# Performance work log

Measured on AMD Instinct MI355X. Metric: run time of the kernel, lower is better.

Reference implementation:

```python
import math
import jax, jax.numpy as jnp
import numpy as np

B, C_S, C_V = 32768, 256, 128
H = max(C_S, C_V)          # c_hidden
RES_B, RES_A = 4, 5        # SO3_Grid(lmax=1, mmax=1): lat=2*(l+1), long=2*l+3
EPS_LN = 1e-5
EPS_V = 1e-5


def _grid_mats():
    # Real spherical harmonics up to l=1 ('integral' normalization, e3nn order
    # [Y00, Y1-1, Y10, Y11] ~ [const, y, z, x]) sampled on a sphere grid, with
    # exact quadrature so from_grid @ to_grid == identity on l<=1 coefficients.
    xb, wb = np.polynomial.legendre.leggauss(RES_B)   # nodes in cos(beta)
    alphas = 2.0 * np.pi * np.arange(RES_A) / RES_A
    wa = 2.0 * np.pi / RES_A
    sb = np.sqrt(1.0 - xb ** 2)
    x = sb[:, None] * np.cos(alphas)[None, :]
    y = sb[:, None] * np.sin(alphas)[None, :]
    z = np.broadcast_to(xb[:, None], (RES_B, RES_A))
    k0 = 0.5 / math.sqrt(math.pi)
    k1 = math.sqrt(3.0 / (4.0 * math.pi))
    Y = np.stack([np.full_like(x, k0), k1 * y, k1 * z, k1 * x], axis=-1)  # [b,a,4]
    to_grid = Y
    from_grid = Y * (wb[:, None, None] * wa)
    return jnp.asarray(to_grid, jnp.float32), jnp.asarray(from_grid, jnp.float32)

TO_GRID, FROM_GRID = _grid_mats()
EXPAND_IDX = jnp.array([0, 1, 1, 1])  # l of each of the (lmax+1)^2=4 coeffs


def _s2_act(x):
    # x: [B, 4, C]; project coeffs to sphere grid, SiLU pointwise, project back
    xg = jnp.einsum('bai,zic->zbac', TO_GRID, x)     # [B, 4, 5, C]
    xg = jax.nn.silu(xg)
    return jnp.einsum('bai,zbac->zic', FROM_GRID, xg)


def _sep_act(x):
    # SeparableS2Activation: SiLU on l=0 scalars, S2 grid activation on full rep
    scalars = jax.nn.silu(x[:, :1, :])
    tensors = _s2_act(x)
    return jnp.concatenate([scalars, tensors[:, 1:, :]], axis=1)


def _layer_norm(x, g, b):
    mu = jnp.mean(x, axis=-1, keepdims=True)
    var = jnp.var(x, axis=-1, keepdims=True)
    return (x - mu) * jax.lax.rsqrt(var + EPS_LN) * g + b


def setup_inputs() -> dict:
    key = jax.random.key(0)
    ks = jax.random.split(key, 8)
    def u(k, shape, fan_in):
        bound = 1.0 / math.sqrt(fan_in)
        return jax.random.uniform(k, shape, jnp.float32, -bound, bound)
    return {
        's': jax.random.normal(ks[0], (B, C_S), jnp.float32),
        'v': jax.random.normal(ks[1], (B, C_V, 3), jnp.float32),
        'Ws': u(ks[2], (H, C_S), C_S),
        'bs': jnp.zeros((H,), jnp.float32),
        'Wv': u(ks[3], (H, C_V), C_V),
        'W2': u(ks[4], (2, H, H), H),
        'b2': jnp.zeros((H,), jnp.float32),
        'Wos': u(ks[5], (C_S, H), H),
        'bos': jnp.zeros((C_S,), jnp.float32),
        'Wov': u(ks[6], (C_V, H), H),
        'gamma_s': jnp.ones((C_S,), jnp.float32),
        'beta_s': jnp.zeros((C_S,), jnp.float32),
        'gamma_v': jnp.ones((C_V,), jnp.float32),
    }


def reference(s, v, Ws, bs, Wv, W2, b2, Wos, bos, Wov, gamma_s, beta_s, gamma_v):
    # embed scalar and vector channels into shared hidden width H
    embed_s = s @ Ws.T + bs                                    # [B, H]
    embed_v = jnp.einsum('bmc,hc->bmh', jnp.swapaxes(v, -1, -2), Wv)  # [B,3,H]
    emb = jnp.concatenate([embed_s[:, None, :], embed_v], axis=1)     # [B,4,H]

    emb = _sep_act(emb)

    # Lmax1_LinearV2: per-l weight expanded over m via index_select, plus l=0 bias
    w_exp = W2[EXPAND_IDX]                                     # [4, H, H]
    emb = jnp.einsum('bmi,moi->bmo', emb, w_exp)
    emb = jnp.concatenate([emb[:, :1] + b2, emb[:, 1:]], axis=1)

    emb = _sep_act(emb)

    out_s = emb[:, 0] @ Wos.T + bos                            # [B, c_s]
    out_v = jnp.einsum('bmh,ch->bmc', emb[:, 1:], Wov)         # [B, 3, c_v]

    out_s = _layer_norm(s + out_s, gamma_s, beta_s)

    # residual + equivariant vector layer norm (NormSO3, l=1 branch only)
    vres = jnp.swapaxes(v, -1, -2) + out_v                     # [B, 3, c_v]
    inv = jax.lax.rsqrt(
        jnp.mean(jnp.sum(vres * vres, axis=1, keepdims=True), axis=2, keepdims=True)
        + EPS_V)
    out_v_final = jnp.swapaxes(vres * inv * gamma_v, -1, -2)   # [B, c_v, 3]
    return out_s, out_v_final
```

## Files before the change

### kernel.cpp

```cpp
#include <hip/hip_runtime.h>
#include <math.h>

#define NT 512
#define BR 16
#define NROWS 32768

typedef __attribute__((ext_vector_type(8))) short bf16x8;
typedef __attribute__((ext_vector_type(4))) float f32x4;
typedef __attribute__((ext_vector_type(2))) float f32x2;
typedef __attribute__((ext_vector_type(2))) unsigned int u32x2;

__device__ __forceinline__ unsigned pk2(float a, float b){
  unsigned ua = __float_as_uint(a); ua += 0x7FFFu + ((ua>>16)&1u);
  unsigned ub = __float_as_uint(b); ub += 0x7FFFu + ((ub>>16)&1u);
  return (ua>>16) | (ub & 0xFFFF0000u);
}
__device__ __forceinline__ unsigned short bf1(float a){
  unsigned ua = __float_as_uint(a); ua += 0x7FFFu + ((ua>>16)&1u);
  return (unsigned short)(ua>>16);
}

__device__ __forceinline__ float exp2_fast(float x){
#if __has_builtin(__builtin_amdgcn_exp2f)
  return __builtin_amdgcn_exp2f(x);
#else
  float r; asm("v_exp_f32 %0, %1" : "=v"(r) : "v"(x)); return r;
#endif
}
__device__ __forceinline__ float rcp_fast(float x){
#if __has_builtin(__builtin_amdgcn_rcpf)
  return __builtin_amdgcn_rcpf(x);
#else
  float r; asm("v_rcp_f32 %0, %1" : "=v"(r) : "v"(x)); return r;
#endif
}

__device__ __forceinline__ f32x2 v2(float x){ f32x2 r; r.x = x; r.y = x; return r; }
__device__ __forceinline__ f32x2 fma2(f32x2 a, f32x2 b, f32x2 c){
  return __builtin_elementwise_fma(a, b, c);
}

#define MFMA(a,b,c) __builtin_amdgcn_mfma_f32_16x16x32_bf16((a),(b),(c),0,0,0)

__global__ void prep_weights(const float* __restrict__ Ws, const float* __restrict__ Wv,
                             const float* __restrict__ W2, const float* __restrict__ Wos,
                             const float* __restrict__ Wov, unsigned short* __restrict__ o){
  int i = blockIdx.x*512 + threadIdx.x;
  if (i >= 327680) return;
  float val;
  if (i < 65536)       val = Ws[i];
  else if (i < 98304)  val = Wv[i-65536];
  else if (i < 229376) val = W2[i-98304];
  else if (i < 294912) val = Wos[i-229376];
  else                 val = Wov[i-294912];
  o[i] = bf1(val);
}

__device__ __forceinline__ void s2act2(f32x2 x0, f32x2 x1, f32x2 x2, f32x2 x3,
                                       f32x2 yy[4]){
  {
    f32x2 xn = v2(-1.44269504f) * x0;
    f32x2 e; e.x = exp2_fast(xn.x); e.y = exp2_fast(xn.y);
    f32x2 den = e + v2(1.0f);
    f32x2 r; r.x = rcp_fast(den.x); r.y = rcp_fast(den.y);
    yy[0] = x0 * r;
  }
  f32x2 t   = v2(-0.40697676f) * x0;
  f32x2 cb0 = fma2(v2( 0.60701885f), x2, t);
  f32x2 cb1 = fma2(v2( 0.23965414f), x2, t);
  f32x2 cb2 = fma2(v2(-0.23965414f), x2, t);
  f32x2 cb3 = fma2(v2(-0.60701885f), x2, t);
  f32x2 d1o = v2(-0.35835520f) * x1, d3o = v2(-0.35835520f) * x3;
  f32x2 d1i = v2(-0.66291491f) * x1, d3i = v2(-0.66291491f) * x3;
  f32x2 a1 = v2(0.f), a2 = v2(0.f), a3 = v2(0.f);
#define PT(xh_expr, S1, S2, S3) { \
    f32x2 xh = (xh_expr); \
    f32x2 e; e.x = exp2_fast(xh.x); e.y = exp2_fast(xh.y); \
    f32x2 den = e + v2(1.0f); \
    f32x2 r; r.x = rcp_fast(den.x); r.y = rcp_fast(den.y); \
    f32x2 u = xh * r; \
    a1 = fma2(v2(S1), u, a1); \
    a2 = fma2(v2(S2), u, a2); \
    a3 = fma2(v2(S3), u, a3); }
#define PT0(xh_expr, S2, S3) { \
    f32x2 xh = (xh_expr); \
    f32x2 e; e.x = exp2_fast(xh.x); e.y = exp2_fast(xh.y); \
    f32x2 den = e + v2(1.0f); \
    f32x2 r; r.x = rcp_fast(den.x); r.y = rcp_fast(den.y); \
    f32x2 u = xh * r; \
    a2 = fma2(v2(S2), u, a2); \
    a3 = fma2(v2(S3), u, a3); }
#define RING(cb, d1, d3, WZ, A1, A2, B0, B1, B2) \
  PT0(cb + d3, WZ, B0) \
  PT(fma2(v2( 0.30901699f), d3, fma2(v2( 0.95105652f), d1, cb)),  A1, WZ,  B1) \
  PT(fma2(v2(-0.80901699f), d3, fma2(v2( 0.58778525f), d1, cb)),  A2, WZ, -(B2)) \
  PT(fma2(v2(-0.80901699f), d3, fma2(v2(-0.58778525f), d1, cb)), -(A2), WZ, -(B2)) \
  PT(fma2(v2( 0.30901699f), d3, fma2(v2(-0.95105652f), d1, cb)), -(A1), WZ,  B1)
  RING(cb0, d1o, d3o,  0.12748554f, -0.07157788f, -0.04423758f, -0.07526144f, -0.02325707f, -0.06088778f)
  RING(cb1, d1i, d3i,  0.09436044f, -0.24823853f, -0.15341984f, -0.26101343f, -0.08065758f, -0.21116430f)
  RING(cb2, d1i, d3i, -0.09436044f, -0.24823853f, -0.15341984f, -0.26101343f, -0.08065758f, -0.21116430f)
  RING(cb3, d1o, d3o, -0.12748554f, -0.07157788f, -0.04423758f, -0.07526144f, -0.02325707f, -0.06088778f)
#undef RING
#undef PT
#undef PT0
  yy[1] = a1; yy[2] = a2; yy[3] = a3;
}

__device__ __forceinline__ void sep_store(const f32x4 (&acc)[4][2],
                                          char* smem, int w, int l16, int lq){
#pragma unroll
  for (int ht2=0; ht2<2; ++ht2){
    f32x2 Y[4][2];
#pragma unroll
    for (int jp=0; jp<2; ++jp){
      f32x2 x0,x1,x2,x3;
      x0.x = acc[0][ht2][2*jp]; x0.y = acc[0][ht2][2*jp+1];
      x1.x = acc[1][ht2][2*jp]; x1.y = acc[1][ht2][2*jp+1];
      x2.x = acc[2][ht2][2*jp]; x2.y = acc[2][ht2][2*jp+1];
      x3.x = acc[3][ht2][2*jp]; x3.y = acc[3][ht2][2*jp+1];
      f32x2 yy[4];
      s2act2(x0,x1,x2,x3, yy);
#pragma unroll
      for (int m=0;m<4;++m) Y[m][jp] = yy[m];
    }
    int h0 = 32*w + 16*ht2 + 4*lq;
#pragma unroll
    for (int m=0;m<4;++m){
      u32x2 p; p.x = pk2(Y[m][0].x, Y[m][0].y); p.y = pk2(Y[m][1].x, Y[m][1].y);
      int off = (l16*2048 + m*512 + h0*2) ^ ((l16&7)<<4);
      *(u32x2*)(smem + off) = p;
    }
  }
}

__global__ void __launch_bounds__(NT, 4) nt_fused(
    const float* __restrict__ s, const float* __restrict__ v,
    const unsigned short* __restrict__ wbf,
    const float* __restrict__ bs, const float* __restrict__ b2,
    const float* __restrict__ bos,
    const float* __restrict__ gamma_s, const float* __restrict__ beta_s,
    const float* __restrict__ gamma_v,
    float* __restrict__ out)
{
  __shared__ __align__(128) char smem[32768];
  const int tid = threadIdx.x;
  const int w = tid >> 6;
  const int lane = tid & 63;
  const int l16 = lane & 15, lq = lane >> 4;
  const int row0 = blockIdx.x * BR;

#pragma unroll
  for (int it=0; it<2; ++it){
    int i = tid + it*512;
    int r = i >> 6, c = (i & 63) * 4;
    f32x4 fv = *(const f32x4*)(s + (size_t)(row0+r)*256 + c);
    u32x2 p; p.x = pk2(fv[0], fv[1]); p.y = pk2(fv[2], fv[3]);
    int off = (r*512 + c*2) ^ ((r&7)<<4);
    *(u32x2*)(smem + off) = p;
  }
#pragma unroll
  for (int it=0; it<3; ++it){
    int i = tid + it*512;
    int r = i / 96, fb = (i % 96) * 4;
    f32x4 fv = *(const f32x4*)(v + (size_t)(row0+r)*384 + fb);
#pragma unroll
    for (int k2=0;k2<4;++k2){
      int flat = fb + k2;
      int c = flat/3, m3 = flat%3;
      int off = 8192 + ((r*768 + m3*256 + c*2) ^ ((r&7)<<4));
      *(unsigned short*)(smem + off) = bf1(fv[k2]);
    }
  }
  __syncthreads();

  const unsigned short* Ws  = wbf;
  const unsigned short* Wv  = wbf + 65536;
  const unsigned short* W20 = wbf + 98304;
  const unsigned short* W21 = wbf + 163840;
  const unsigned short* Wos = wbf + 229376;
  const unsigned short* Wov = wbf + 294912;

  const f32x4 zero = {0.f,0.f,0.f,0.f};
  f32x4 acc[4][2];
#pragma unroll
  for (int m=0;m<4;++m){ acc[m][0]=zero; acc[m][1]=zero; }

  {
    const int h0 = 32*w + l16, h1 = h0 + 16;
#pragma unroll
    for (int ks=0;ks<8;++ks){
      int k = ks*32 + lq*8;
      bf16x8 a0 = *(const bf16x8*)(Ws + h0*256 + k);
      bf16x8 a1 = *(const bf16x8*)(Ws + h1*256 + k);
      bf16x8 b  = *(const bf16x8*)(smem + ((l16*512 + k*2) ^ ((l16&7)<<4)));
      acc[0][0] = MFMA(a0,b,acc[0][0]);
      acc[0][1] = MFMA(a1,b,acc[0][1]);
    }
#pragma unroll
    for (int ks=0;ks<4;++ks){
      int k = ks*32 + lq*8;
      bf16x8 a0 = *(const bf16x8*)(Wv + (32*w + l16)*128 + k);
      bf16x8 a1 = *(const bf16x8*)(Wv + (32*w + 16 + l16)*128 + k);
#pragma unroll
      for (int m3=0;m3<3;++m3){
        bf16x8 b = *(const bf16x8*)(smem + (8192 + ((l16*768 + m3*256 + k*2) ^ ((l16&7)<<4))));
        acc[1+m3][0] = MFMA(a0,b,acc[1+m3][0]);
        acc[1+m3][1] = MFMA(a1,b,acc[1+m3][1]);
      }
    }
  }
  acc[0][0] += *(const f32x4*)(bs + 32*w + 4*lq);
  acc[0][1] += *(const f32x4*)(bs + 32*w + 16 + 4*lq);

  __syncthreads();
  sep_store(acc, smem, w, l16, lq);
  __syncthreads();

  f32x4 acc2[4][2];
#pragma unroll
  for (int m=0;m<4;++m){ acc2[m][0]=zero; acc2[m][1]=zero; }
  {
    const int h0 = 32*w + l16, h1 = h0 + 16;
#pragma unroll
    for (int ks=0;ks<8;++ks){
      int k = ks*32 + lq*8;
      bf16x8 a00 = *(const bf16x8*)(W20 + h0*256 + k);
      bf16x8 a01 = *(const bf16x8*)(W20 + h1*256 + k);
      bf16x8 a10 = *(const bf16x8*)(W21 + h0*256 + k);
      bf16x8 a11 = *(const bf16x8*)(W21 + h1*256 + k);
#pragma unroll
      for (int m=0;m<4;++m){
        bf16x8 b = *(const bf16x8*)(smem + ((l16*2048 + m*512 + k*2) ^ ((l16&7)<<4)));
        acc2[m][0] = MFMA((m==0)?a00:a10, b, acc2[m][0]);
        acc2[m][1] = MFMA((m==0)?a01:a11, b, acc2[m][1]);
      }
    }
  }
  acc2[0][0] += *(const f32x4*)(b2 + 32*w + 4*lq);
  acc2[0][1] += *(const f32x4*)(b2 + 32*w + 16 + 4*lq);

  __syncthreads();
  sep_store(acc2, smem, w, l16, lq);
  __syncthreads();

  f32x4 accS[2]; accS[0]=zero; accS[1]=zero;
  f32x4 accV[3]; accV[0]=zero; accV[1]=zero; accV[2]=zero;
  {
    const int hs0 = 32*w + l16, hs1 = hs0 + 16;
    const int hv  = 16*w + l16;
#pragma unroll
    for (int ks=0;ks<8;++ks){
      int k = ks*32 + lq*8;
      bf16x8 as0 = *(const bf16x8*)(Wos + hs0*256 + k);
      bf16x8 as1 = *(const bf16x8*)(Wos + hs1*256 + k);
      bf16x8 av  = *(const bf16x8*)(Wov + hv*256 + k);
      bf16x8 b0  = *(const bf16x8*)(smem + ((l16*2048 + 0*512 + k*2) ^ ((l16&7)<<4)));
      accS[0] = MFMA(as0,b0,accS[0]);
      accS[1] = MFMA(as1,b0,accS[1]);
#pragma unroll
      for (int m3=0;m3<3;++m3){
        bf16x8 bm = *(const bf16x8*)(smem + ((l16*2048 + (1+m3)*512 + k*2) ^ ((l16&7)<<4)));
        accV[m3] = MFMA(av, bm, accV[m3]);
      }
    }
  }
  accS[0] += *(const f32x4*)(bos + 32*w + 4*lq);
  accS[1] += *(const f32x4*)(bos + 32*w + 16 + 4*lq);

  __syncthreads();
  {
    float* scr = (float*)smem;
    *(f32x4*)(scr + l16*260 + 32*w + 4*lq)      = accS[0];
    *(f32x4*)(scr + l16*260 + 32*w + 16 + 4*lq) = accS[1];
  }
  __syncthreads();
  {
    int rr = tid >> 5, g = tid & 31, c0 = g*8;
    const float* srow = s + (size_t)(row0+rr)*256 + c0;
    f32x4 s0 = *(const f32x4*)srow, s1 = *(const f32x4*)(srow+4);
    const float* scr = (const float*)smem + rr*260 + c0;
    f32x4 o0 = *(const f32x4*)scr, o1 = *(const f32x4*)(scr+4);
    float xv[8]; float sum=0.f, sq=0.f;
#pragma unroll
    for (int k2=0;k2<4;++k2){ xv[k2]=s0[k2]+o0[k2]; xv[4+k2]=s1[k2]+o1[k2]; }
#pragma unroll
    for (int k2=0;k2<8;++k2){ sum += xv[k2]; sq += xv[k2]*xv[k2]; }
#pragma unroll
    for (int mk=1; mk<32; mk<<=1){ sum += __shfl_xor(sum, mk, 64); sq += __shfl_xor(sq, mk, 64); }
    float mu = sum*(1.0f/256.0f);
    float var = sq*(1.0f/256.0f) - mu*mu;
    float rs = rsqrtf(var + 1e-5f);
    f32x4 ga = *(const f32x4*)(gamma_s+c0), gb = *(const f32x4*)(gamma_s+c0+4);
    f32x4 ba = *(const f32x4*)(beta_s+c0),  bb = *(const f32x4*)(beta_s+c0+4);
    f32x4 r0, r1;
#pragma unroll
    for (int k2=0;k2<4;++k2){
      r0[k2] = (xv[k2]  -mu)*rs*ga[k2] + ba[k2];
      r1[k2] = (xv[4+k2]-mu)*rs*gb[k2] + bb[k2];
    }
    float* orow = out + (size_t)(row0+rr)*256 + c0;
    *(f32x4*)orow = r0; *(f32x4*)(orow+4) = r1;
  }
  __syncthreads();
  {
    float* scr = (float*)smem;
#pragma unroll
    for (int m3=0;m3<3;++m3)
      *(f32x4*)(scr + l16*388 + m3*128 + 16*w + 4*lq) = accV[m3];
  }
  __syncthreads();
  {
    int rr = tid >> 5, g = tid & 31, c0 = g*4;
    const float* vrow = v + (size_t)(row0+rr)*384 + c0*3;
    f32x4 vv0 = *(const f32x4*)(vrow);
    f32x4 vv1 = *(const f32x4*)(vrow+4);
    f32x4 vv2 = *(const f32x4*)(vrow+8);
    const float* scr = (const float*)smem + rr*388;
    float vr[12]; float ss = 0.f;
#pragma unroll
    for (int f=0; f<12; ++f){
      int k = f/3, m3 = f%3;
      float base = (f<4) ? vv0[f] : ((f<8) ? vv1[f-4] : vv2[f-8]);
      float val = base + scr[m3*128 + c0 + k];
      vr[f] = val; ss += val*val;
    }
#pragma unroll
    for (int mk=1; mk<32; mk<<=1) ss += __shfl_xor(ss, mk, 64);
    float inv = rsqrtf(ss*(1.0f/128.0f) + 1e-5f);
    f32x4 gvv = *(const f32x4*)(gamma_v + c0);
    f32x4 o0, o1, o2;
#pragma unroll
    for (int f=0; f<12; ++f){
      float val = vr[f]*inv*gvv[f/3];
      if (f<4) o0[f]=val; else if (f<8) o1[f-4]=val; else o2[f-8]=val;
    }
    float* orow = out + (size_t)NROWS*256 + (size_t)(row0+rr)*384 + c0*3;
    *(f32x4*)(orow) = o0; *(f32x4*)(orow+4) = o1; *(f32x4*)(orow+8) = o2;
  }
}

extern "C" void kernel_launch(void* const* d_in, const int* in_sizes, int n_in,
                              void* d_out, int out_size, void* d_ws, size_t ws_size,
                              hipStream_t stream)
{
  const float* s   = (const float*)d_in[0];
  const float* v   = (const float*)d_in[1];
  const float* Ws  = (const float*)d_in[2];
  const float* bs  = (const float*)d_in[3];
  const float* Wv  = (const float*)d_in[4];
  const float* W2  = (const float*)d_in[5];
  const float* b2  = (const float*)d_in[6];
  const float* Wos = (const float*)d_in[7];
  const float* bos = (const float*)d_in[8];
  const float* Wov = (const float*)d_in[9];
  const float* gs  = (const float*)d_in[10];
  const float* bts = (const float*)d_in[11];
  const float* gv  = (const float*)d_in[12];
  float* out = (float*)d_out;
  unsigned short* wbf = (unsigned short*)d_ws;

  prep_weights<<<640, 512, 0, stream>>>(Ws, Wv, W2, Wos, Wov, wbf);
  nt_fused<<<NROWS/BR, NT, 0, stream>>>(s, v, wbf, bs, b2, bos, gs, bts, gv, out);
}
```

Baseline: 211.9 us.

## Process 32 rows per block, reusing each weight fragment across two row tiles

Doubles the rows handled per block from 16 to 32. Each loaded bf16 weight fragment now feeds MFMAs for two 16-row batch tiles, which halves weight traffic per row from global memory and L2. In exchange it doubles the accumulator registers and LDS use (64KB), which may lower occupancy under the launch bounds of 4 and could cause register spills.

```diff
diff --git a/kernel.cpp b/kernel.cpp
--- a/kernel.cpp
+++ b/kernel.cpp
@@ -2,7 +2,7 @@
 #include <math.h>
 
 #define NT 512
-#define BR 16
+#define BR 32
 #define NROWS 32768
 
 typedef __attribute__((ext_vector_type(8))) short bf16x8;
@@ -106,29 +106,34 @@
   yy[1] = a1; yy[2] = a2; yy[3] = a3;
 }
 
-__device__ __forceinline__ void sep_store(const f32x4 (&acc)[4][2],
+__device__ __forceinline__ void sep_store(const f32x4 (&acc)[4][2][2],
                                           char* smem, int w, int l16, int lq){
-#pragma unroll
-  for (int ht2=0; ht2<2; ++ht2){
-    f32x2 Y[4][2];
-#pragma unroll
-    for (int jp=0; jp<2; ++jp){
-      f32x2 x0,x1,x2,x3;
-      x0.x = acc[0][ht2][2*jp]; x0.y = acc[0][ht2][2*jp+1];
-      x1.x = acc[1][ht2][2*jp]; x1.y = acc[1][ht2][2*jp+1];
-      x2.x = acc[2][ht2][2*jp]; x2.y = acc[2][ht2][2*jp+1];
-      x3.x = acc[3][ht2][2*jp]; x3.y = acc[3][ht2][2*jp+1];
-      f32x2 yy[4];
-      s2act2(x0,x1,x2,x3, yy);
-#pragma unroll
-      for (int m=0;m<4;++m) Y[m][jp] = yy[m];
-    }
-    int h0 = 32*w + 16*ht2 + 4*lq;
-#pragma unroll
-    for (int m=0;m<4;++m){
-      u32x2 p; p.x = pk2(Y[m][0].x, Y[m][0].y); p.y = pk2(Y[m][1].x, Y[m][1].y);
-      int off = (l16*2048 + m*512 + h0*2) ^ ((l16&7)<<4);
-      *(u32x2*)(smem + off) = p;
+  const int sw = (l16 & 7) << 4;
+#pragma unroll
+  for (int bt=0; bt<2; ++bt){
+#pragma unroll
+    for (int hj=0; hj<2; ++hj){
+      f32x2 Y[4][2];
+#pragma unroll
+      for (int jp=0; jp<2; ++jp){
+        f32x2 x0,x1,x2,x3;
+        x0.x = acc[0][hj][bt][2*jp]; x0.y = acc[0][hj][bt][2*jp+1];
+        x1.x = acc[1][hj][bt][2*jp]; x1.y = acc[1][hj][bt][2*jp+1];
+        x2.x = acc[2][hj][bt][2*jp]; x2.y = acc[2][hj][bt][2*jp+1];
+        x3.x = acc[3][hj][bt][2*jp]; x3.y = acc[3][hj][bt][2*jp+1];
+        f32x2 yy[4];
+        s2act2(x0,x1,x2,x3, yy);
+#pragma unroll
+        for (int m=0;m<4;++m) Y[m][jp] = yy[m];
+      }
+      int r  = bt*16 + l16;
+      int h0 = 32*w + hj*16 + 4*lq;
+#pragma unroll
+      for (int m=0;m<4;++m){
+        u32x2 p; p.x = pk2(Y[m][0].x, Y[m][0].y); p.y = pk2(Y[m][1].x, Y[m][1].y);
+        int off = (r*2048 + m*512 + h0*2) ^ sw;
+        *(u32x2*)(smem + off) = p;
+      }
     }
   }
 }
@@ -142,15 +147,16 @@
     const float* __restrict__ gamma_v,
     float* __restrict__ out)
 {
-  __shared__ __align__(128) char smem[32768];
+  __shared__ __align__(128) char smem[65536];
   const int tid = threadIdx.x;
   const int w = tid >> 6;
   const int lane = tid & 63;
   const int l16 = lane & 15, lq = lane >> 4;
+  const int sw = (l16 & 7) << 4;
   const int row0 = blockIdx.x * BR;
 
 #pragma unroll
-  for (int it=0; it<2; ++it){
+  for (int it=0; it<4; ++it){
     int i = tid + it*512;
     int r = i >> 6, c = (i & 63) * 4;
     f32x4 fv = *(const f32x4*)(s + (size_t)(row0+r)*256 + c);
@@ -159,7 +165,7 @@
     *(u32x2*)(smem + off) = p;
   }
 #pragma unroll
-  for (int it=0; it<3; ++it){
+  for (int it=0; it<6; ++it){
     int i = tid + it*512;
     int r = i / 96, fb = (i % 96) * 4;
     f32x4 fv = *(const f32x4*)(v + (size_t)(row0+r)*384 + fb);
@@ -167,7 +173,7 @@
     for (int k2=0;k2<4;++k2){
       int flat = fb + k2;
       int c = flat/3, m3 = flat%3;
-      int off = 8192 + ((r*768 + m3*256 + c*2) ^ ((r&7)<<4));
+      int off = 16384 + ((r*768 + m3*256 + c*2) ^ ((r&7)<<4));
       *(unsigned short*)(smem + off) = bf1(fv[k2]);
     }
   }
@@ -180,102 +186,136 @@
   const unsigned short* Wos = wbf + 229376;
   const unsigned short* Wov = wbf + 294912;
 
+  const int hA = 32*w + l16;
   const f32x4 zero = {0.f,0.f,0.f,0.f};
-  f32x4 acc[4][2];
-#pragma unroll
-  for (int m=0;m<4;++m){ acc[m][0]=zero; acc[m][1]=zero; }
-
-  {
-    const int h0 = 32*w + l16, h1 = h0 + 16;
+  f32x4 acc[4][2][2];
+#pragma unroll
+  for (int m=0;m<4;++m)
+#pragma unroll
+    for (int hj=0;hj<2;++hj){ acc[m][hj][0]=zero; acc[m][hj][1]=zero; }
+
+  {
 #pragma unroll
     for (int ks=0;ks<8;++ks){
       int k = ks*32 + lq*8;
-      bf16x8 a0 = *(const bf16x8*)(Ws + h0*256 + k);
-      bf16x8 a1 = *(const bf16x8*)(Ws + h1*256 + k);
-      bf16x8 b  = *(const bf16x8*)(smem + ((l16*512 + k*2) ^ ((l16&7)<<4)));
-      acc[0][0] = MFMA(a0,b,acc[0][0]);
-      acc[0][1] = MFMA(a1,b,acc[0][1]);
+      bf16x8 a0 = *(const bf16x8*)(Ws + hA*256 + k);
+      bf16x8 a1 = *(const bf16x8*)(Ws + (hA+16)*256 + k);
+#pragma unroll
+      for (int bt=0;bt<2;++bt){
+        bf16x8 b = *(const bf16x8*)(smem + (((bt*16+l16)*512 + k*2) ^ sw));
+        acc[0][0][bt] = MFMA(a0,b,acc[0][0][bt]);
+        acc[0][1][bt] = MFMA(a1,b,acc[0][1][bt]);
+      }
     }
 #pragma unroll
     for (int ks=0;ks<4;++ks){
       int k = ks*32 + lq*8;
-      bf16x8 a0 = *(const bf16x8*)(Wv + (32*w + l16)*128 + k);
-      bf16x8 a1 = *(const bf16x8*)(Wv + (32*w + 16 + l16)*128 + k);
-#pragma unroll
-      for (int m3=0;m3<3;++m3){
-        bf16x8 b = *(const bf16x8*)(smem + (8192 + ((l16*768 + m3*256 + k*2) ^ ((l16&7)<<4))));
-        acc[1+m3][0] = MFMA(a0,b,acc[1+m3][0]);
-        acc[1+m3][1] = MFMA(a1,b,acc[1+m3][1]);
-      }
-    }
-  }
-  acc[0][0] += *(const f32x4*)(bs + 32*w + 4*lq);
-  acc[0][1] += *(const f32x4*)(bs + 32*w + 16 + 4*lq);
+      bf16x8 a0 = *(const bf16x8*)(Wv + hA*128 + k);
+      bf16x8 a1 = *(const bf16x8*)(Wv + (hA+16)*128 + k);
+#pragma unroll
+      for (int m3=0;m3<3;++m3)
+#pragma unroll
+        for (int bt=0;bt<2;++bt){
+          bf16x8 b = *(const bf16x8*)(smem + (16384 + (((bt*16+l16)*768 + m3*256 + k*2) ^ sw)));
+          acc[1+m3][0][bt] = MFMA(a0,b,acc[1+m3][0][bt]);
+          acc[1+m3][1][bt] = MFMA(a1,b,acc[1+m3][1][bt]);
+        }
+    }
+  }
+  {
+    f32x4 bs0 = *(const f32x4*)(bs + 32*w + 4*lq);
+    f32x4 bs1 = *(const f32x4*)(bs + 32*w + 16 + 4*lq);
+#pragma unroll
+    for (int bt=0;bt<2;++bt){ acc[0][0][bt] += bs0; acc[0][1][bt] += bs1; }
+  }
 
   __syncthreads();
   sep_store(acc, smem, w, l16, lq);
   __syncthreads();
 
-  f32x4 acc2[4][2];
-#pragma unroll
-  for (int m=0;m<4;++m){ acc2[m][0]=zero; acc2[m][1]=zero; }
-  {
-    const int h0 = 32*w + l16, h1 = h0 + 16;
+  f32x4 acc2[4][2][2];
+#pragma unroll
+  for (int m=0;m<4;++m)
+#pragma unroll
+    for (int hj=0;hj<2;++hj){ acc2[m][hj][0]=zero; acc2[m][hj][1]=zero; }
+  {
 #pragma unroll
     for (int ks=0;ks<8;++ks){
       int k = ks*32 + lq*8;
-      bf16x8 a00 = *(const bf16x8*)(W20 + h0*256 + k);
-      bf16x8 a01 = *(const bf16x8*)(W20 + h1*256 + k);
-      bf16x8 a10 = *(const bf16x8*)(W21 + h0*256 + k);
-      bf16x8 a11 = *(const bf16x8*)(W21 + h1*256 + k);
-#pragma unroll
-      for (int m=0;m<4;++m){
-        bf16x8 b = *(const bf16x8*)(smem + ((l16*2048 + m*512 + k*2) ^ ((l16&7)<<4)));
-        acc2[m][0] = MFMA((m==0)?a00:a10, b, acc2[m][0]);
-        acc2[m][1] = MFMA((m==0)?a01:a11, b, acc2[m][1]);
-      }
-    }
-  }
-  acc2[0][0] += *(const f32x4*)(b2 + 32*w + 4*lq);
-  acc2[0][1] += *(const f32x4*)(b2 + 32*w + 16 + 4*lq);
+      bf16x8 a00 = *(const bf16x8*)(W20 + hA*256 + k);
+      bf16x8 a01 = *(const bf16x8*)(W20 + (hA+16)*256 + k);
+      bf16x8 a10 = *(const bf16x8*)(W21 + hA*256 + k);
+      bf16x8 a11 = *(const bf16x8*)(W21 + (hA+16)*256 + k);
+#pragma unroll
+      for (int m=0;m<4;++m)
+#pragma unroll
+        for (int bt=0;bt<2;++bt){
+          bf16x8 b = *(const bf16x8*)(smem + (((bt*16+l16)*2048 + m*512 + k*2) ^ sw));
+          acc2[m][0][bt] = MFMA((m==0)?a00:a10, b, acc2[m][0][bt]);
+          acc2[m][1][bt] = MFMA((m==0)?a01:a11, b, acc2[m][1][bt]);
+        }
+    }
+  }
+  {
+    f32x4 b20 = *(const f32x4*)(b2 + 32*w + 4*lq);
+    f32x4 b21 = *(const f32x4*)(b2 + 32*w + 16 + 4*lq);
+#pragma unroll
+    for (int bt=0;bt<2;++bt){ acc2[0][0][bt] += b20; acc2[0][1][bt] += b21; }
+  }
 
   __syncthreads();
   sep_store(acc2, smem, w, l16, lq);
   __syncthreads();
 
-  f32x4 accS[2]; accS[0]=zero; accS[1]=zero;
-  f32x4 accV[3]; accV[0]=zero; accV[1]=zero; accV[2]=zero;
-  {
-    const int hs0 = 32*w + l16, hs1 = hs0 + 16;
-    const int hv  = 16*w + l16;
+  f32x4 accS[2][2]; f32x4 accV[3][2];
+#pragma unroll
+  for (int bt=0;bt<2;++bt){
+    accS[0][bt]=zero; accS[1][bt]=zero;
+    accV[0][bt]=zero; accV[1][bt]=zero; accV[2][bt]=zero;
+  }
+  {
+    const int hv = 16*w + l16;
 #pragma unroll
     for (int ks=0;ks<8;++ks){
       int k = ks*32 + lq*8;
-      bf16x8 as0 = *(const bf16x8*)(Wos + hs0*256 + k);
-      bf16x8 as1 = *(const bf16x8*)(Wos + hs1*256 + k);
+      bf16x8 as0 = *(const bf16x8*)(Wos + hA*256 + k);
+      bf16x8 as1 = *(const bf16x8*)(Wos + (hA+16)*256 + k);
       bf16x8 av  = *(const bf16x8*)(Wov + hv*256 + k);
-      bf16x8 b0  = *(const bf16x8*)(smem + ((l16*2048 + 0*512 + k*2) ^ ((l16&7)<<4)));
-      accS[0] = MFMA(as0,b0,accS[0]);
-      accS[1] = MFMA(as1,b0,accS[1]);
-#pragma unroll
-      for (int m3=0;m3<3;++m3){
-        bf16x8 bm = *(const bf16x8*)(smem + ((l16*2048 + (1+m3)*512 + k*2) ^ ((l16&7)<<4)));
-        accV[m3] = MFMA(av, bm, accV[m3]);
+#pragma unroll
+      for (int bt=0;bt<2;++bt){
+        int rb = (bt*16+l16)*2048;
+        bf16x8 b0 = *(const bf16x8*)(smem + ((rb + k*2) ^ sw));
+        accS[0][bt] = MFMA(as0,b0,accS[0][bt]);
+        accS[1][bt] = MFMA(as1,b0,accS[1][bt]);
+#pragma unroll
+        for (int m3=0;m3<3;++m3){
+          bf16x8 bm = *(const bf16x8*)(smem + ((rb + (1+m3)*512 + k*2) ^ sw));
+          accV[m3][bt] = MFMA(av, bm, accV[m3][bt]);
+        }
       }
     }
   }
-  accS[0] += *(const f32x4*)(bos + 32*w + 4*lq);
-  accS[1] += *(const f32x4*)(bos + 32*w + 16 + 4*lq);
+  {
+    f32x4 bo0 = *(const f32x4*)(bos + 32*w + 4*lq);
+    f32x4 bo1 = *(const f32x4*)(bos + 32*w + 16 + 4*lq);
+#pragma unroll
+    for (int bt=0;bt<2;++bt){ accS[0][bt] += bo0; accS[1][bt] += bo1; }
+  }
 
   __syncthreads();
   {
     float* scr = (float*)smem;
-    *(f32x4*)(scr + l16*260 + 32*w + 4*lq)      = accS[0];
-    *(f32x4*)(scr + l16*260 + 32*w + 16 + 4*lq) = accS[1];
-  }
-  __syncthreads();
-  {
-    int rr = tid >> 5, g = tid & 31, c0 = g*8;
+#pragma unroll
+    for (int bt=0;bt<2;++bt){
+      int r = bt*16 + l16;
+      *(f32x4*)(scr + r*260 + 32*w + 4*lq)      = accS[0][bt];
+      *(f32x4*)(scr + r*260 + 32*w + 16 + 4*lq) = accS[1][bt];
+    }
+  }
+  __syncthreads();
+#pragma unroll
+  for (int h=0; h<2; ++h){
+    int rr = h*16 + (tid >> 5), g = tid & 31, c0 = g*8;
     const float* srow = s + (size_t)(row0+rr)*256 + c0;
     f32x4 s0 = *(const f32x4*)srow, s1 = *(const f32x4*)(srow+4);
     const float* scr = (const float*)smem + rr*260 + c0;
@@ -305,12 +345,17 @@
   {
     float* scr = (float*)smem;
 #pragma unroll
-    for (int m3=0;m3<3;++m3)
-      *(f32x4*)(scr + l16*388 + m3*128 + 16*w + 4*lq) = accV[m3];
-  }
-  __syncthreads();
-  {
-    int rr = tid >> 5, g = tid & 31, c0 = g*4;
+    for (int bt=0;bt<2;++bt){
+      int r = bt*16 + l16;
+#pragma unroll
+      for (int m3=0;m3<3;++m3)
+        *(f32x4*)(scr + r*388 + m3*128 + 16*w + 4*lq) = accV[m3][bt];
+    }
+  }
+  __syncthreads();
+#pragma unroll
+  for (int h=0; h<2; ++h){
+    int rr = h*16 + (tid >> 5), g = tid & 31, c0 = g*4;
     const float* vrow = v + (size_t)(row0+rr)*384 + c0*3;
     f32x4 vv0 = *(const f32x4*)(vrow);
     f32x4 vv1 = *(const f32x4*)(vrow+4);
```

Result: faster. 182.5 us (-13.9%).
